# Performance work log

Hardware: AMD Instinct MI355X
Metric: run time of the kernel (lower is better)

Reference implementation:

```python
import jax, jax.numpy as jnp
import numpy as np

B, N, G = 16, 6000, 256
T = 200                     # TRAIN_ROIS_PER_IMAGE
RATIO = 0.33                # POSITIVE_ROI_RATIO
POS_NUM = int(T * RATIO)    # 66 positive slots
NEG_SLOTS = T - POS_NUM     # 134 negative slots
BBOX_STD = jnp.asarray([0.1, 0.1, 0.2, 0.2], jnp.float32)
EPS = 1e-8


def _rand_boxes(key, b, n):
    # valid [y1,x1,y2,x2] boxes in [0,1]
    k1, k2 = jax.random.split(key)
    tl = jax.random.uniform(k1, (b, n, 2)) * 0.7
    wh = jax.random.uniform(k2, (b, n, 2)) * 0.25 + 0.02
    return jnp.concatenate([tl, tl + wh], axis=-1).astype(jnp.float32)


def setup_inputs() -> dict:
    key = jax.random.key(0)
    k1, k2, k3, k4, k5 = jax.random.split(key, 5)
    rois = _rand_boxes(k1, B, N)
    rois = rois.at[:, N - 1000:].set(0.0)          # zero padding tail (remove_zero_padding)
    gt_boxes = _rand_boxes(k2, B, G)
    gt_ids = jax.random.randint(k3, (B, G), 1, 81, dtype=jnp.int32)
    gt_ids = gt_ids.at[:, G - 32:G - 16].set(-1)   # crowd boxes (ids < 0)
    gt_ids = gt_ids.at[:, G - 16:].set(0)          # padded gt
    gt_boxes = gt_boxes.at[:, G - 16:].set(0.0)
    pos_score = jax.random.uniform(k4, (B, N), dtype=jnp.float32)
    neg_score = jax.random.uniform(k5, (B, N), dtype=jnp.float32)
    return {"rois": rois, "gt_ids": gt_ids, "gt_boxes": gt_boxes,
            "pos_score": pos_score, "neg_score": neg_score}


def _pairwise_iou(a, b):
    # a:[N,4], b:[G,4] -> [N,G]
    y1 = jnp.maximum(a[:, None, 0], b[None, :, 0])
    x1 = jnp.maximum(a[:, None, 1], b[None, :, 1])
    y2 = jnp.minimum(a[:, None, 2], b[None, :, 2])
    x2 = jnp.minimum(a[:, None, 3], b[None, :, 3])
    inter = jnp.clip(y2 - y1, 0.0) * jnp.clip(x2 - x1, 0.0)
    area_a = (a[:, 2] - a[:, 0]) * (a[:, 3] - a[:, 1])
    area_b = (b[:, 2] - b[:, 0]) * (b[:, 3] - b[:, 1])
    union = area_a[:, None] + area_b[None, :] - inter
    return inter / jnp.maximum(union, EPS)


def _bbox_offset(boxes, gt):
    h = jnp.maximum(boxes[:, 2] - boxes[:, 0], EPS)
    w = jnp.maximum(boxes[:, 3] - boxes[:, 1], EPS)
    cy = boxes[:, 0] + 0.5 * h
    cx = boxes[:, 1] + 0.5 * w
    gh = jnp.maximum(gt[:, 2] - gt[:, 0], EPS)
    gw = jnp.maximum(gt[:, 3] - gt[:, 1], EPS)
    gcy = gt[:, 0] + 0.5 * gh
    gcx = gt[:, 1] + 0.5 * gw
    off = jnp.stack([(gcy - cy) / h, (gcx - cx) / w,
                     jnp.log(gh / h), jnp.log(gw / w)], axis=1)
    return off / BBOX_STD


def _per_image(rois, gt_ids, gt_boxes, pos_score, neg_score):
    roi_valid = jnp.any(rois != 0.0, axis=1)        # [N]
    gt_valid = jnp.any(gt_boxes != 0.0, axis=1)     # [G]
    crowd = gt_valid & (gt_ids < 0)
    non_crowd = gt_valid & (gt_ids > 0)

    iou = _pairwise_iou(rois, gt_boxes)             # [N,G]
    iou_nc = jnp.where(non_crowd[None, :], iou, -1.0)
    iou_nc_max = jnp.max(iou_nc, axis=1)
    iou_cr_max = jnp.max(jnp.where(crowd[None, :], iou, 0.0), axis=1)

    pos_mask = roi_valid & (iou_nc_max >= 0.5)
    neg_mask = roi_valid & (iou_nc_max < 0.5) & (iou_cr_max < 0.001)

    # random sampling == sort by iid uniform scores (masked out -> -inf)
    pos_idx = jnp.argsort(-jnp.where(pos_mask, pos_score, -jnp.inf))[:POS_NUM]
    pos_count = jnp.minimum(jnp.sum(pos_mask), POS_NUM).astype(jnp.int32)
    pos_slot_valid = jnp.arange(POS_NUM) < pos_count

    neg_target = (jnp.float32(1.0 / RATIO) * pos_count.astype(jnp.float32)).astype(jnp.int32) - pos_count
    neg_idx = jnp.argsort(-jnp.where(neg_mask, neg_score, -jnp.inf))[:NEG_SLOTS]
    neg_count = jnp.minimum(jnp.sum(neg_mask).astype(jnp.int32),
                            jnp.minimum(neg_target, NEG_SLOTS))
    neg_slot_valid = jnp.arange(NEG_SLOTS) < neg_count

    pos_rois_raw = rois[pos_idx]                                   # [P,4]
    pos_rois = jnp.where(pos_slot_valid[:, None], pos_rois_raw, 0.0)
    neg_rois = jnp.where(neg_slot_valid[:, None], rois[neg_idx], 0.0)

    assign = jnp.argmax(iou_nc[pos_idx], axis=1)                   # gt assignment
    roi_gt_boxes = gt_boxes[assign]
    roi_gt_ids = jnp.where(pos_slot_valid, gt_ids[assign], 0)

    off = _bbox_offset(pos_rois_raw, roi_gt_boxes)
    off = jnp.where(pos_slot_valid[:, None], off, 0.0)

    out_rois = jnp.concatenate([pos_rois, neg_rois], axis=0)       # [T,4]
    out_ids = jnp.pad(roi_gt_ids, (0, NEG_SLOTS))                  # [T]
    out_off = jnp.pad(off, ((0, NEG_SLOTS), (0, 0)))               # [T,4]
    return out_rois, out_ids, out_off


def reference(rois, gt_ids, gt_boxes, pos_score, neg_score):
    return jax.vmap(_per_image)(rois, gt_ids, gt_boxes, pos_score, neg_score)
```

## Files before the change

### kernel.cpp

```cpp
#include <hip/hip_runtime.h>

#define BIMG 16
#define NROI 6000
#define NGT  256
#define TPOS 66
#define TNEG 134
#define TTOT 200
#define EPSF 1e-8f
#define INVALID_SCORE 0xFFFFFFFFu

#define RPB 256
#define UNITSB 24
#define P1_BLOCKS (UNITSB * BIMG)
#define NWAIT (2 * BIMG)
#define NT 256
#define VSLOTS 6
#define CAND_CAP 384

#define MAGIC1 0x9E3779B9u
#define MAGIC2 0x85EBCA77u

typedef unsigned long long u64;
typedef unsigned int u32;
typedef unsigned short u16;

struct P1Shared {
    float4 ncbox[NGT];
    float  ncarea[NGT];
    float4 crbox[NGT];
    float  crarea[NGT];
    u16    gmap[NGT];
    int    wnc[4], wcr[4];
};

struct SelShared {
    u32 hist[2048];
    u32 wtot[4];
    u32 wsuf[4];
    int pick;
    u32 higher;
    u32 pickpop;
    u32 count;
    u64 comp[CAND_CAP];
    int cnt;
    int sel[TNEG];
};

__device__ __forceinline__ void phase1_block(
    int unit,
    const float* __restrict__ rois, const int* __restrict__ gt_ids,
    const float* __restrict__ gt_boxes, const float* __restrict__ pos_score,
    const float* __restrict__ neg_score, u32* __restrict__ pos_s,
    u32* __restrict__ neg_s, u32* __restrict__ assign, u32* __restrict__ flags,
    P1Shared& S)
{
#pragma clang fp contract(off)
    const int b = unit / UNITSB;
    const int u = unit - b * UNITSB;
    const int tid = threadIdx.x;

    const int n = u * RPB + tid;
    const int ne = min(n, NROI - 1);
    const float4 rb = ((const float4*)rois)[b * NROI + ne];
    const float ps_in = pos_score[b * NROI + ne];
    const float ns_in = neg_score[b * NROI + ne];

    {
        const int g = tid;
        const int lane = g & 63, w = g >> 6;
        float4 gb = ((const float4*)gt_boxes)[b * NGT + g];
        bool valid = (gb.x != 0.f) || (gb.y != 0.f) || (gb.z != 0.f) || (gb.w != 0.f);
        int id = gt_ids[b * NGT + g];
        float area = (gb.z - gb.x) * (gb.w - gb.y);
        bool isnc = valid && (id > 0);
        bool iscr = valid && (id < 0);
        u64 mnc = __ballot(isnc);
        u64 mcr = __ballot(iscr);
        if (lane == 0) { S.wnc[w] = (int)__popcll(mnc); S.wcr[w] = (int)__popcll(mcr); }
        __syncthreads();
        int offnc = 0, offcr = 0;
        for (int j = 0; j < w; ++j) { offnc += S.wnc[j]; offcr += S.wcr[j]; }
        u64 below = (lane == 0) ? 0ull : (~0ull >> (64 - lane));
        if (isnc) {
            int slot = offnc + (int)__popcll(mnc & below);
            S.ncbox[slot] = gb;
            S.ncarea[slot] = area;
            S.gmap[slot] = (u16)g;
        }
        if (iscr) {
            int slot = offcr + (int)__popcll(mcr & below);
            S.crbox[slot] = gb;
            S.crarea[slot] = area;
        }
    }
    __syncthreads();
    const int nccnt = S.wnc[0] + S.wnc[1] + S.wnc[2] + S.wnc[3];
    const int crcnt = S.wcr[0] + S.wcr[1] + S.wcr[2] + S.wcr[3];

    const bool rvalid = (rb.x != 0.f) || (rb.y != 0.f) || (rb.z != 0.f) || (rb.w != 0.f);
    float best = -1.0f;
    int   bsl  = 0;
    float crmax = 0.0f;

    if (rvalid) {
        const float area_a = (rb.z - rb.x) * (rb.w - rb.y);
#pragma unroll 4
        for (int i = 0; i < nccnt; ++i) {
            float4 p0 = S.ncbox[i];
            float  ab = S.ncarea[i];
            float y1 = fmaxf(rb.x, p0.x);
            float x1 = fmaxf(rb.y, p0.y);
            float y2 = fminf(rb.z, p0.z);
            float x2 = fminf(rb.w, p0.w);
            float ih = fmaxf(y2 - y1, 0.0f);
            float iw = fmaxf(x2 - x1, 0.0f);
            float inter = ih * iw;
            float uni = fmaxf(area_a + ab - inter, EPSF);
            float iou = inter / uni;
            if (iou > best) { best = iou; bsl = i; }
        }
#pragma unroll 4
        for (int i = 0; i < crcnt; ++i) {
            float4 p0 = S.crbox[i];
            float  ab = S.crarea[i];
            float y1 = fmaxf(rb.x, p0.x);
            float x1 = fmaxf(rb.y, p0.y);
            float y2 = fminf(rb.z, p0.z);
            float x2 = fminf(rb.w, p0.w);
            float ih = fmaxf(y2 - y1, 0.0f);
            float iw = fmaxf(x2 - x1, 0.0f);
            float inter = ih * iw;
            float uni = fmaxf(area_a + ab - inter, EPSF);
            crmax = fmaxf(crmax, inter / uni);
        }
    }

    if (n < NROI) {
        u32 ps = INVALID_SCORE, ns = INVALID_SCORE;
        if (rvalid) {
            if (best >= 0.5f)
                ps = __float_as_uint(ps_in);
            if ((best < 0.5f) && (crmax < 0.001f))
                ns = __float_as_uint(ns_in);
        }
        int gsel = (nccnt > 0) ? (int)S.gmap[bsl] : 0;
        __hip_atomic_store(&pos_s[b * NROI + n], ps,
                           __ATOMIC_RELAXED, __HIP_MEMORY_SCOPE_AGENT);
        __hip_atomic_store(&neg_s[b * NROI + n], ns,
                           __ATOMIC_RELAXED, __HIP_MEMORY_SCOPE_AGENT);
        __hip_atomic_store(&assign[b * NROI + n], (u32)gsel,
                           __ATOMIC_RELAXED, __HIP_MEMORY_SCOPE_AGENT);
    }

    __syncthreads();
    if (tid == 0) {
        __hip_atomic_store(&flags[2 * unit],     MAGIC1,
                           __ATOMIC_RELAXED, __HIP_MEMORY_SCOPE_AGENT);
        __hip_atomic_store(&flags[2 * unit + 1], MAGIC2,
                           __ATOMIC_RELAXED, __HIP_MEMORY_SCOPE_AGENT);
    }
}

__device__ __forceinline__ int count_valid(const u32* __restrict__ src,
                                           int tid, int lane, SelShared* S)
{
    const uint4* src4 = (const uint4*)src;
    int myvalid = 0;
#pragma unroll
    for (int s = 0; s < VSLOTS; ++s) {
        int vi = s * NT + tid;
        uint4 v = src4[vi];
        int base = vi * 4;
        myvalid += (base + 0 < NROI && v.x != INVALID_SCORE);
        myvalid += (base + 1 < NROI && v.y != INVALID_SCORE);
        myvalid += (base + 2 < NROI && v.z != INVALID_SCORE);
        myvalid += (base + 3 < NROI && v.w != INVALID_SCORE);
    }
    for (int off = 1; off < 64; off <<= 1) myvalid += __shfl_xor(myvalid, off);
    if (tid == 0) S->count = 0;
    __syncthreads();
    if (lane == 0) atomicAdd(&S->count, (u32)myvalid);
    __syncthreads();
    int tot = (int)S->count;
    __syncthreads();
    return tot;
}

__device__ __forceinline__ int radix_select(const u32* __restrict__ src, int K,
                                            int tid, int lane, int w, SelShared* S)
{
    const uint4* src4 = (const uint4*)src;
    int myvalid = 0;
#pragma unroll
    for (int s = 0; s < VSLOTS; ++s) {
        int vi = s * NT + tid;
        uint4 v = src4[vi];
        int base = vi * 4;
        myvalid += (base + 0 < NROI && v.x != INVALID_SCORE);
        myvalid += (base + 1 < NROI && v.y != INVALID_SCORE);
        myvalid += (base + 2 < NROI && v.z != INVALID_SCORE);
        myvalid += (base + 3 < NROI && v.w != INVALID_SCORE);
    }
    for (int off = 1; off < 64; off <<= 1) myvalid += __shfl_xor(myvalid, off);
    if (tid == 0) S->count = 0;
    __syncthreads();
    if (lane == 0) atomicAdd(&S->count, (u32)myvalid);
    __syncthreads();
    const int total = (int)S->count;
    const int K0 = min(K, total);
    if (K0 <= 0) return total;

    int Krem = K0;
    u64 prefix = 0ull, mask = 0ull;
    int cand = total;

    for (int p = 3; p >= 0; --p) {
        if (cand <= CAND_CAP) break;
        const int shift = p * 11;
        for (int i = tid; i < 2048; i += NT) S->hist[i] = 0;
        __syncthreads();
#pragma unroll
        for (int s = 0; s < VSLOTS; ++s) {
            int vi = s * NT + tid;
            uint4 v = src4[vi];
            int base = vi * 4;
            u32 vv[4] = {v.x, v.y, v.z, v.w};
#pragma unroll
            for (int j = 0; j < 4; ++j) {
                int idx = base + j;
                if (idx < NROI && vv[j] != INVALID_SCORE) {
                    u64 kk = ((u64)vv[j] << 13) | (u64)(8191 - idx);
                    if ((kk & mask) == prefix)
                        atomicAdd(&S->hist[(u32)(kk >> shift) & 2047u], 1u);
                }
            }
        }
        __syncthreads();
        u32 local = 0;
#pragma unroll
        for (int j = 0; j < 8; ++j) local += S->hist[8 * tid + j];
        u32 suf = local;
        for (int off = 1; off < 64; off <<= 1) {
            u32 v = __shfl_down(suf, off);
            if (lane + off < 64) suf += v;
        }
        if (lane == 0) S->wtot[w] = suf;
        __syncthreads();
        if (tid < 4) {
            u32 t = 0;
            for (int j = tid + 1; j < 4; ++j) t += S->wtot[j];
            S->wsuf[tid] = t;
        }
        __syncthreads();
        u32 Sincl = suf + S->wsuf[w];
        for (int k2 = 0; k2 < 8; ++k2) {
            u32 h = S->hist[8 * tid + k2];
            u32 Snext = Sincl - h;
            if (Sincl >= (u32)Krem && Snext < (u32)Krem) {
                S->pick = 8 * tid + k2;
                S->higher = Snext;
                S->pickpop = h;
            }
            Sincl = Snext;
        }
        __syncthreads();
        prefix |= ((u64)(u32)S->pick) << shift;
        mask   |= (2047ull << shift);
        Krem   -= (int)S->higher;
        cand    = (K0 - Krem) + (int)S->pickpop;
        __syncthreads();
    }

    if (tid == 0) S->cnt = 0;
    __syncthreads();
#pragma unroll
    for (int s = 0; s < VSLOTS; ++s) {
        int vi = s * NT + tid;
        uint4 v = src4[vi];
        int base = vi * 4;
        u32 vv[4] = {v.x, v.y, v.z, v.w};
#pragma unroll
        for (int j = 0; j < 4; ++j) {
            int idx = base + j;
            if (idx < NROI && vv[j] != INVALID_SCORE) {
                u64 kk = ((u64)vv[j] << 13) | (u64)(8191 - idx);
                if ((kk & mask) >= prefix) {
                    int pos = atomicAdd(&S->cnt, 1);
                    S->comp[pos] = kk;
                }
            }
        }
    }
    __syncthreads();
    const int Cnt = S->cnt;
    for (int c0 = tid; c0 < Cnt; c0 += NT) {
        u64 kk = S->comp[c0];
        int rank = 0;
        for (int j = 0; j < Cnt; ++j) rank += (S->comp[j] > kk);
        if (rank < K0) S->sel[rank] = 8191 - (int)(kk & 8191ull);
    }
    __syncthreads();
    return total;
}

__device__ __forceinline__ void phase2_block(
    int wbid,
    const float* __restrict__ rois, const int* __restrict__ gt_ids,
    const float* __restrict__ gt_boxes, const u32* __restrict__ pos_s,
    const u32* __restrict__ neg_s, const u32* __restrict__ assign,
    const u32* __restrict__ flags, float* __restrict__ out, SelShared& S)
{
#pragma clang fp contract(off)
    __shared__ int s_ndone;
    const int b = wbid >> 1;
    const int side = wbid & 1;
    const int tid = threadIdx.x;
    const int lane = tid & 63;
    const int w = tid >> 6;

    const u32* fb = flags + 2 * (b * UNITSB);
    int mydone = (tid < UNITSB) ? 0 : 1;
    for (;;) {
        if (tid == 0) s_ndone = 0;
        __syncthreads();
        if (!mydone) {
            u32 a = __hip_atomic_load(&fb[2 * tid],
                                      __ATOMIC_RELAXED, __HIP_MEMORY_SCOPE_AGENT);
            u32 c = __hip_atomic_load(&fb[2 * tid + 1],
                                      __ATOMIC_RELAXED, __HIP_MEMORY_SCOPE_AGENT);
            mydone = (a == MAGIC1 && c == MAGIC2);
        }
        int d = mydone;
        for (int off = 1; off < 64; off <<= 1) d += __shfl_xor(d, off);
        if (lane == 0) atomicAdd(&s_ndone, d);
        __syncthreads();
        if (s_ndone == NT) break;
        __builtin_amdgcn_s_sleep(8);
    }
    if (tid == 0)
        (void)__hip_atomic_load(&fb[0], __ATOMIC_ACQUIRE, __HIP_MEMORY_SCOPE_AGENT);
    __syncthreads();

    float* out_rois = out;
    float* out_ids  = out + BIMG * TTOT * 4;
    float* out_off  = out + BIMG * TTOT * 4 + BIMG * TTOT;

    if (side == 0) {
        const int pos_total = radix_select(pos_s + (size_t)b * NROI, TPOS,
                                           tid, lane, w, &S);
        const int pos_count = min(pos_total, TPOS);

        if (tid < TPOS) {
            const int base = b * TTOT + tid;
            float4 ro  = make_float4(0.f, 0.f, 0.f, 0.f);
            float  idv = 0.f;
            float4 off = make_float4(0.f, 0.f, 0.f, 0.f);
            if (tid < pos_count) {
                int nn = S.sel[tid];
                float4 rb = ((const float4*)rois)[b * NROI + nn];
                ro = rb;
                int g = (int)assign[b * NROI + nn];
                float4 gb = ((const float4*)gt_boxes)[b * NGT + g];
                idv = (float)gt_ids[b * NGT + g];

                float h  = fmaxf(rb.z - rb.x, EPSF);
                float wd = fmaxf(rb.w - rb.y, EPSF);
                float cy = rb.x + 0.5f * h;
                float cx = rb.y + 0.5f * wd;
                float gh = fmaxf(gb.z - gb.x, EPSF);
                float gw = fmaxf(gb.w - gb.y, EPSF);
                float gcy = gb.x + 0.5f * gh;
                float gcx = gb.y + 0.5f * gw;
                off.x = ((gcy - cy) / h)  / 0.1f;
                off.y = ((gcx - cx) / wd) / 0.1f;
                off.z = logf(gh / h)  / 0.2f;
                off.w = logf(gw / wd) / 0.2f;
            }
            ((float4*)out_rois)[base] = ro;
            out_ids[base] = idv;
            ((float4*)out_off)[base] = off;
        }
    } else {
        const int pos_total = count_valid(pos_s + (size_t)b * NROI, tid, lane, &S);
        const int pos_count = min(pos_total, TPOS);
        const float ratio_inv = (float)(1.0 / 0.33);
        const int neg_target = (int)(ratio_inv * (float)pos_count) - pos_count;

        const int neg_total = radix_select(neg_s + (size_t)b * NROI, TNEG,
                                           tid, lane, w, &S);
        const int neg_count = max(0, min(neg_total, min(neg_target, TNEG)));

        if (tid < TNEG) {
            const int base = b * TTOT + TPOS + tid;
            float4 ro = make_float4(0.f, 0.f, 0.f, 0.f);
            if (tid < neg_count) {
                int nn = S.sel[tid];
                ro = ((const float4*)rois)[b * NROI + nn];
            }
            ((float4*)out_rois)[base] = ro;
            out_ids[base] = 0.f;
            ((float4*)out_off)[base] = make_float4(0.f, 0.f, 0.f, 0.f);
        }
    }
}

__global__ __launch_bounds__(NT, 4)
void fused_kernel(const float* __restrict__ rois,
                  const int* __restrict__ gt_ids,
                  const float* __restrict__ gt_boxes,
                  const float* __restrict__ pos_score,
                  const float* __restrict__ neg_score,
                  u32* __restrict__ pos_s,
                  u32* __restrict__ neg_s,
                  u32* __restrict__ assign,
                  u32* __restrict__ flags,
                  float* __restrict__ out)
{
    constexpr size_t SB = sizeof(P1Shared) > sizeof(SelShared)
                        ? sizeof(P1Shared) : sizeof(SelShared);
    __shared__ __align__(16) char smem[SB];

    if (blockIdx.x >= NWAIT) {
        phase1_block((int)blockIdx.x - NWAIT, rois, gt_ids, gt_boxes, pos_score,
                     neg_score, pos_s, neg_s, assign, flags,
                     *reinterpret_cast<P1Shared*>(smem));
    } else {
        phase2_block((int)blockIdx.x, rois, gt_ids, gt_boxes,
                     pos_s, neg_s, assign, flags, out,
                     *reinterpret_cast<SelShared*>(smem));
    }
}

extern "C" void kernel_launch(void* const* d_in, const int* in_sizes, int n_in,
                              void* d_out, int out_size, void* d_ws, size_t ws_size,
                              hipStream_t stream) {
    const float* rois      = (const float*)d_in[0];
    const int*   gt_ids    = (const int*)d_in[1];
    const float* gt_boxes  = (const float*)d_in[2];
    const float* pos_score = (const float*)d_in[3];
    const float* neg_score = (const float*)d_in[4];
    float* out = (float*)d_out;

    char* ws = (char*)d_ws;
    u32* pos_s  = (u32*)(ws + 0);
    u32* neg_s  = (u32*)(ws + 384000);
    u32* assign = (u32*)(ws + 768000);
    u32* flags  = (u32*)(ws + 1152000);

    fused_kernel<<<NWAIT + P1_BLOCKS, NT, 0, stream>>>(
        rois, gt_ids, gt_boxes, pos_score, neg_score,
        pos_s, neg_s, assign, flags, out);
}
```

Measured before the change: 101.6 us.

## Split IoU scan across thread pairs, pass positive counts through flags, pad rank loop

Phase 1 now assigns two threads per ROI, each scanning half of the non-crowd and crowd GT lists and merging with a lane shuffle. RPB drops to 128, which roughly doubles the phase-1 block count. Each block counts its positives and encodes the count into its completion flags, so the selection blocks get the positive total without rescanning pos_s (count_valid is removed). The candidate rank loop is zero-padded to a multiple of 16 and unrolled. In exchange, the flag encoding is more complex, and ca<=RPB is used as a validity check on it.

After: 94.33 us. 1.08x faster.

```diff
diff --git a/kernel.cpp b/kernel.cpp
--- a/kernel.cpp
+++ b/kernel.cpp
@@ -9,8 +9,8 @@
 #define EPSF 1e-8f
 #define INVALID_SCORE 0xFFFFFFFFu
 
-#define RPB 256
-#define UNITSB 24
+#define RPB 128
+#define UNITSB 47
 #define P1_BLOCKS (UNITSB * BIMG)
 #define NWAIT (2 * BIMG)
 #define NT 256
@@ -31,6 +31,7 @@
     float  crarea[NGT];
     u16    gmap[NGT];
     int    wnc[4], wcr[4];
+    int    poscnt;
 };
 
 struct SelShared {
@@ -58,12 +59,19 @@
     const int b = unit / UNITSB;
     const int u = unit - b * UNITSB;
     const int tid = threadIdx.x;
-
-    const int n = u * RPB + tid;
+    const int sub = tid & 1;
+    const int r   = tid >> 1;
+
+    if (tid == 0) S.poscnt = 0;
+
+    const int n = u * RPB + r;
     const int ne = min(n, NROI - 1);
     const float4 rb = ((const float4*)rois)[b * NROI + ne];
-    const float ps_in = pos_score[b * NROI + ne];
-    const float ns_in = neg_score[b * NROI + ne];
+    float ps_in = 0.f, ns_in = 0.f;
+    if (sub == 0) {
+        ps_in = pos_score[b * NROI + ne];
+        ns_in = neg_score[b * NROI + ne];
+    }
 
     {
         const int g = tid;
@@ -104,8 +112,11 @@
 
     if (rvalid) {
         const float area_a = (rb.z - rb.x) * (rb.w - rb.y);
+        const int h  = nccnt >> 1;
+        const int i0 = sub ? h : 0;
+        const int i1 = sub ? nccnt : h;
 #pragma unroll 4
-        for (int i = 0; i < nccnt; ++i) {
+        for (int i = i0; i < i1; ++i) {
             float4 p0 = S.ncbox[i];
             float  ab = S.ncarea[i];
             float y1 = fmaxf(rb.x, p0.x);
@@ -119,8 +130,11 @@
             float iou = inter / uni;
             if (iou > best) { best = iou; bsl = i; }
         }
+        const int hc  = crcnt >> 1;
+        const int c0i = sub ? hc : 0;
+        const int c1i = sub ? crcnt : hc;
 #pragma unroll 4
-        for (int i = 0; i < crcnt; ++i) {
+        for (int i = c0i; i < c1i; ++i) {
             float4 p0 = S.crbox[i];
             float  ab = S.crarea[i];
             float y1 = fmaxf(rb.x, p0.x);
@@ -133,16 +147,25 @@
             float uni = fmaxf(area_a + ab - inter, EPSF);
             crmax = fmaxf(crmax, inter / uni);
         }
-    }
-
-    if (n < NROI) {
-        u32 ps = INVALID_SCORE, ns = INVALID_SCORE;
-        if (rvalid) {
-            if (best >= 0.5f)
-                ps = __float_as_uint(ps_in);
-            if ((best < 0.5f) && (crmax < 0.001f))
-                ns = __float_as_uint(ns_in);
-        }
+        float ov = __shfl_xor(best, 1);
+        int   os = __shfl_xor(bsl, 1);
+        float oc = __shfl_xor(crmax, 1);
+        if ((ov > best) || ((ov == best) && (os < bsl))) { best = ov; bsl = os; }
+        crmax = fmaxf(crmax, oc);
+    }
+
+    u32 ps = INVALID_SCORE, ns = INVALID_SCORE;
+    if (rvalid && n < NROI) {
+        if (best >= 0.5f)
+            ps = __float_as_uint(ps_in);
+        if ((best < 0.5f) && (crmax < 0.001f))
+            ns = __float_as_uint(ns_in);
+    }
+    {
+        u64 pb = __ballot((sub == 0) && (ps != INVALID_SCORE));
+        if ((tid & 63) == 0) atomicAdd(&S.poscnt, (int)__popcll(pb));
+    }
+    if (sub == 0 && n < NROI) {
         int gsel = (nccnt > 0) ? (int)S.gmap[bsl] : 0;
         __hip_atomic_store(&pos_s[b * NROI + n], ps,
                            __ATOMIC_RELAXED, __HIP_MEMORY_SCOPE_AGENT);
@@ -154,36 +177,12 @@
 
     __syncthreads();
     if (tid == 0) {
-        __hip_atomic_store(&flags[2 * unit],     MAGIC1,
+        u32 cnt = (u32)S.poscnt;
+        __hip_atomic_store(&flags[2 * unit],     MAGIC1 ^ cnt,
                            __ATOMIC_RELAXED, __HIP_MEMORY_SCOPE_AGENT);
-        __hip_atomic_store(&flags[2 * unit + 1], MAGIC2,
+        __hip_atomic_store(&flags[2 * unit + 1], MAGIC2 ^ cnt,
                            __ATOMIC_RELAXED, __HIP_MEMORY_SCOPE_AGENT);
     }
-}
-
-__device__ __forceinline__ int count_valid(const u32* __restrict__ src,
-                                           int tid, int lane, SelShared* S)
-{
-    const uint4* src4 = (const uint4*)src;
-    int myvalid = 0;
-#pragma unroll
-    for (int s = 0; s < VSLOTS; ++s) {
-        int vi = s * NT + tid;
-        uint4 v = src4[vi];
-        int base = vi * 4;
-        myvalid += (base + 0 < NROI && v.x != INVALID_SCORE);
-        myvalid += (base + 1 < NROI && v.y != INVALID_SCORE);
-        myvalid += (base + 2 < NROI && v.z != INVALID_SCORE);
-        myvalid += (base + 3 < NROI && v.w != INVALID_SCORE);
-    }
-    for (int off = 1; off < 64; off <<= 1) myvalid += __shfl_xor(myvalid, off);
-    if (tid == 0) S->count = 0;
-    __syncthreads();
-    if (lane == 0) atomicAdd(&S->count, (u32)myvalid);
-    __syncthreads();
-    int tot = (int)S->count;
-    __syncthreads();
-    return tot;
 }
 
 __device__ __forceinline__ int radix_select(const u32* __restrict__ src, int K,
@@ -293,10 +292,18 @@
     }
     __syncthreads();
     const int Cnt = S->cnt;
+    const int CntP = (Cnt + 15) & ~15;
+    for (int i = Cnt + tid; i < CntP; i += NT) S->comp[i] = 0ull;
+    __syncthreads();
     for (int c0 = tid; c0 < Cnt; c0 += NT) {
         u64 kk = S->comp[c0];
         int rank = 0;
-        for (int j = 0; j < Cnt; ++j) rank += (S->comp[j] > kk);
+        for (int j = 0; j < CntP; j += 16) {
+            int r16 = 0;
+#pragma unroll
+            for (int q = 0; q < 16; ++q) r16 += (S->comp[j + q] > kk);
+            rank += r16;
+        }
         if (rank < K0) S->sel[rank] = 8191 - (int)(kk & 8191ull);
     }
     __syncthreads();
@@ -312,6 +319,7 @@
 {
 #pragma clang fp contract(off)
     __shared__ int s_ndone;
+    __shared__ int s_psum;
     const int b = wbid >> 1;
     const int side = wbid & 1;
     const int tid = threadIdx.x;
@@ -320,6 +328,7 @@
 
     const u32* fb = flags + 2 * (b * UNITSB);
     int mydone = (tid < UNITSB) ? 0 : 1;
+    int mycnt = 0;
     for (;;) {
         if (tid == 0) s_ndone = 0;
         __syncthreads();
@@ -328,7 +337,8 @@
                                       __ATOMIC_RELAXED, __HIP_MEMORY_SCOPE_AGENT);
             u32 c = __hip_atomic_load(&fb[2 * tid + 1],
                                       __ATOMIC_RELAXED, __HIP_MEMORY_SCOPE_AGENT);
-            mydone = (a == MAGIC1 && c == MAGIC2);
+            u32 ca = a ^ MAGIC1, cb = c ^ MAGIC2;
+            if (ca == cb && ca <= (u32)RPB) { mydone = 1; mycnt = (int)ca; }
         }
         int d = mydone;
         for (int off = 1; off < 64; off <<= 1) d += __shfl_xor(d, off);
@@ -337,17 +347,21 @@
         if (s_ndone == NT) break;
         __builtin_amdgcn_s_sleep(8);
     }
-    if (tid == 0)
+    if (tid == 0) {
         (void)__hip_atomic_load(&fb[0], __ATOMIC_ACQUIRE, __HIP_MEMORY_SCOPE_AGENT);
-    __syncthreads();
+        s_psum = 0;
+    }
+    __syncthreads();
+    if (tid < UNITSB && mycnt) atomicAdd(&s_psum, mycnt);
+    __syncthreads();
+    const int pos_total = s_psum;
 
     float* out_rois = out;
     float* out_ids  = out + BIMG * TTOT * 4;
     float* out_off  = out + BIMG * TTOT * 4 + BIMG * TTOT;
 
     if (side == 0) {
-        const int pos_total = radix_select(pos_s + (size_t)b * NROI, TPOS,
-                                           tid, lane, w, &S);
+        radix_select(pos_s + (size_t)b * NROI, TPOS, tid, lane, w, &S);
         const int pos_count = min(pos_total, TPOS);
 
         if (tid < TPOS) {
@@ -381,7 +395,6 @@
             ((float4*)out_off)[base] = off;
         }
     } else {
-        const int pos_total = count_valid(pos_s + (size_t)b * NROI, tid, lane, &S);
         const int pos_count = min(pos_total, TPOS);
         const float ratio_inv = (float)(1.0 / 0.33);
         const int neg_target = (int)(ratio_inv * (float)pos_count) - pos_count;
```
